# Optimization experiments

Measured on AMD Instinct MI355X. Metric: run time of the kernel, lower is better.

## Reference

```python
import jax, jax.numpy as jnp
import numpy as np

INPUT_SIZE = 1024
HIDDEN_SIZE = 1024
BATCH = 8192


def setup_inputs() -> dict:
    key = jax.random.key(0)
    ks = jax.random.split(key, 10)
    H, I, B = HIDDEN_SIZE, INPUT_SIZE, BATCH
    s = 1.0 / np.sqrt(H)  # scale params so activations stay in sane range
    return {
        "input": jax.random.normal(ks[0], (B, I), jnp.float32),
        "hx": jax.random.normal(ks[1], (B, H), jnp.float32),
        "cx": jax.random.normal(ks[2], (B, H), jnp.float32),
        "att": jax.random.normal(ks[3], (B, I), jnp.float32),
        "weight_ih": jax.random.normal(ks[4], (4 * H, I), jnp.float32) * s,
        "weight_hh": jax.random.normal(ks[5], (4 * H, H), jnp.float32) * s,
        "bias_ih": jax.random.normal(ks[6], (4 * H,), jnp.float32),
        "bias_hh": jax.random.normal(ks[7], (4 * H,), jnp.float32),
        "weight_att": jax.random.normal(ks[8], (2 * H, I), jnp.float32) * s,
        "bias_att": jax.random.normal(ks[9], (2 * H,), jnp.float32),
    }


def reference(input, hx, cx, att, weight_ih, weight_hh, bias_ih, bias_hh,
              weight_att, bias_att):
    H = weight_hh.shape[1]
    # gates: [B, 4H]
    gates = input @ weight_ih.T + bias_ih + hx @ weight_hh.T + bias_hh
    att_gates = att @ weight_att.T + bias_att  # [B, 2H]
    ingate, forgetgate, cellgate, outgate = jnp.split(gates, 4, axis=1)
    ingate_att, attgate = jnp.split(att_gates, 2, axis=1)
    ingate = jax.nn.sigmoid(ingate)
    forgetgate = jax.nn.sigmoid(forgetgate)
    cellgate = jnp.tanh(cellgate)
    ingate_att = jax.nn.sigmoid(ingate_att)
    attgate = jnp.tanh(attgate)
    outgate = jax.nn.sigmoid(outgate)
    cy = forgetgate * cx + ingate * cellgate + ingate_att * attgate
    hy = outgate * jnp.tanh(cy)
    return (hy, cy)
```

## Files before the change

kernel.cpp:

```cpp
#include <hip/hip_runtime.h>


typedef __attribute__((ext_vector_type(8))) __bf16 bf16x8;
typedef __attribute__((ext_vector_type(8))) unsigned short ushort8;
typedef __attribute__((ext_vector_type(4))) float f32x4;

#define AS1 __attribute__((address_space(1)))
#define AS3 __attribute__((address_space(3)))

__device__ __forceinline__ void gld16(const unsigned short* g, unsigned short* l) {
    __builtin_amdgcn_global_load_lds((const AS1 void*)g, (AS3 void*)l, 16, 0, 0);
}

__device__ __forceinline__ unsigned short f2bf(float f) {
    unsigned int u = __builtin_bit_cast(unsigned int, f);
    u += 0x7fffu + ((u >> 16) & 1u);
    return (unsigned short)(u >> 16);
}

__device__ __forceinline__ float sigmoidf_(float x) { return 1.f / (1.f + __expf(-x)); }
__device__ __forceinline__ float tanhf_(float x) {
    float e = __expf(-2.f * fabsf(x));
    float t = (1.f - e) / (1.f + e);
    return x >= 0.f ? t : -t;
}

__device__ __forceinline__ bf16x8 ldfrag(const unsigned short* p) {
    return __builtin_bit_cast(bf16x8, *(const ushort8*)p);
}

__global__ void cast_all_k(const float* __restrict__ input, const float* __restrict__ hx,
                           const float* __restrict__ att,   const float* __restrict__ w_ih,
                           const float* __restrict__ w_hh,  const float* __restrict__ w_att,
                           const float* __restrict__ b_ih,  const float* __restrict__ b_hh,
                           unsigned short* __restrict__ XH, unsigned short* __restrict__ ATTb,
                           unsigned short* __restrict__ W4, unsigned short* __restrict__ WA,
                           float* __restrict__ bias4)
{
    int gid = blockIdx.x * blockDim.x + threadIdx.x;
    if (gid < 4096) bias4[gid] = b_ih[gid] + b_hh[gid];
    const int total = 8912896;
    for (int i = gid; i < total; i += gridDim.x * blockDim.x) {
        const float* src; unsigned short* dst; int ld, off, rel;
        if (i < 2097152)      { src = input; dst = XH;   ld = 2048; off = 0;    rel = i; }
        else if (i < 4194304) { src = hx;    dst = XH;   ld = 2048; off = 1024; rel = i - 2097152; }
        else if (i < 6291456) { src = att;   dst = ATTb; ld = 1024; off = 0;    rel = i - 4194304; }
        else if (i < 7340032) { src = w_ih;  dst = W4;   ld = 2048; off = 0;    rel = i - 6291456; }
        else if (i < 8388608) { src = w_hh;  dst = W4;   ld = 2048; off = 1024; rel = i - 7340032; }
        else                  { src = w_att; dst = WA;   ld = 1024; off = 0;    rel = i - 8388608; }
        int e = rel * 4;
        int r = e >> 10, c = e & 1023;
        const float4 v = *(const float4*)(src + e);
        ushort4 p;
        p.x = f2bf(v.x); p.y = f2bf(v.y); p.z = f2bf(v.z); p.w = f2bf(v.w);
        *(ushort4*)(dst + r * ld + off + c) = p;
    }
}

__global__ __launch_bounds__(256, 2) void att_gemm_k(
    const unsigned short* __restrict__ ATT, const unsigned short* __restrict__ WA,
    const float* __restrict__ bias_att, float* __restrict__ attprod)
{
    __shared__ unsigned short As[128 * 32];
    __shared__ unsigned short Bs[128 * 32];
    const int tid  = threadIdx.x;
    const int wave = tid >> 6, lane = tid & 63;
    const int l15 = lane & 15, quad = lane >> 4;
    const int row0 = blockIdx.x * 128;
    const int n0   = blockIdx.y * 64;

    f32x4 acc[2][8];
    const f32x4 z = {0.f, 0.f, 0.f, 0.f};
#pragma unroll
    for (int i = 0; i < 2; ++i)
#pragma unroll
        for (int j = 0; j < 8; ++j) acc[i][j] = z;

    const int ar = tid >> 2;
    const int kp_sw = (tid & 3) ^ ((ar >> 1) & 3);
    const unsigned short* aG0 = ATT + (row0 + ar) * 1024 + kp_sw * 8;
    const unsigned short* aG1 = aG0 + 64 * 1024;
    const unsigned short* bG0 = WA + (n0 + ar) * 1024 + kp_sw * 8;
    const unsigned short* bG1 = WA + (1024 + n0 + ar) * 1024 + kp_sw * 8;
    unsigned short* aL0 = As + tid * 8;  unsigned short* aL1 = As + (tid + 256) * 8;
    unsigned short* bL0 = Bs + tid * 8;  unsigned short* bL1 = Bs + (tid + 256) * 8;

    const int sw8 = (quad ^ ((l15 >> 1) & 3)) * 8;
    const int aoff0 = (wave * 32 + l15) * 32 + sw8;
    const int aoff1 = aoff0 + 16 * 32;

    for (int kt = 0; kt < 32; ++kt) {
        gld16(aG0, aL0); gld16(aG1, aL1);
        gld16(bG0, bL0); gld16(bG1, bL1);
        aG0 += 32; aG1 += 32; bG0 += 32; bG1 += 32;
        __syncthreads();
        bf16x8 a0 = ldfrag(As + aoff0);
        bf16x8 a1 = ldfrag(As + aoff1);
#pragma unroll
        for (int cf = 0; cf < 8; ++cf) {
            bf16x8 b = ldfrag(Bs + (cf * 16 + l15) * 32 + sw8);
            acc[0][cf] = __builtin_amdgcn_mfma_f32_16x16x32_bf16(a0, b, acc[0][cf], 0, 0, 0);
            acc[1][cf] = __builtin_amdgcn_mfma_f32_16x16x32_bf16(a1, b, acc[1][cf], 0, 0, 0);
        }
        __syncthreads();
    }

    const int Rbase = row0 + wave * 32 + quad * 4;
#pragma unroll
    for (int rf = 0; rf < 2; ++rf)
#pragma unroll
        for (int jf = 0; jf < 4; ++jf) {
            int col = n0 + jf * 16 + l15;
            float b0 = bias_att[col], b1 = bias_att[1024 + col];
#pragma unroll
            for (int reg = 0; reg < 4; ++reg) {
                int R = Rbase + rf * 16 + reg;
                float ia = sigmoidf_(acc[rf][jf][reg] + b0);
                float ag = tanhf_(acc[rf][4 + jf][reg] + b1);
                attprod[R * 1024 + col] = ia * ag;
            }
        }
}

__global__ __launch_bounds__(256, 2) void main_gemm_k(
    const unsigned short* __restrict__ XH, const unsigned short* __restrict__ W4,
    const float* __restrict__ bias4, const float* __restrict__ attprod,
    const float* __restrict__ cx, float* __restrict__ out)
{
    __shared__ unsigned short As[128 * 32];
    __shared__ unsigned short Bs[128 * 32];
    const int tid  = threadIdx.x;
    const int wave = tid >> 6, lane = tid & 63;
    const int l15 = lane & 15, quad = lane >> 4;
    const int row0 = blockIdx.x * 128;
    const int n0   = blockIdx.y * 32;

    f32x4 acc[2][8];
    const f32x4 z = {0.f, 0.f, 0.f, 0.f};
#pragma unroll
    for (int i = 0; i < 2; ++i)
#pragma unroll
        for (int j = 0; j < 8; ++j) acc[i][j] = z;

    const int ar = tid >> 2;
    const int kp_sw = (tid & 3) ^ ((ar >> 1) & 3);
    const unsigned short* aG0 = XH + (row0 + ar) * 2048 + kp_sw * 8;
    const unsigned short* aG1 = aG0 + 64 * 2048;
    const unsigned short* bG0 = W4 + ((ar >> 5) * 1024 + n0 + (ar & 31)) * 2048 + kp_sw * 8;
    const unsigned short* bG1 = bG0 + 2 * 1024 * 2048;
    unsigned short* aL0 = As + tid * 8;  unsigned short* aL1 = As + (tid + 256) * 8;
    unsigned short* bL0 = Bs + tid * 8;  unsigned short* bL1 = Bs + (tid + 256) * 8;

    const int sw8 = (quad ^ ((l15 >> 1) & 3)) * 8;
    const int aoff0 = (wave * 32 + l15) * 32 + sw8;
    const int aoff1 = aoff0 + 16 * 32;

    for (int kt = 0; kt < 64; ++kt) {
        gld16(aG0, aL0); gld16(aG1, aL1);
        gld16(bG0, bL0); gld16(bG1, bL1);
        aG0 += 32; aG1 += 32; bG0 += 32; bG1 += 32;
        __syncthreads();
        bf16x8 a0 = ldfrag(As + aoff0);
        bf16x8 a1 = ldfrag(As + aoff1);
#pragma unroll
        for (int cf = 0; cf < 8; ++cf) {
            bf16x8 b = ldfrag(Bs + (cf * 16 + l15) * 32 + sw8);
            acc[0][cf] = __builtin_amdgcn_mfma_f32_16x16x32_bf16(a0, b, acc[0][cf], 0, 0, 0);
            acc[1][cf] = __builtin_amdgcn_mfma_f32_16x16x32_bf16(a1, b, acc[1][cf], 0, 0, 0);
        }
        __syncthreads();
    }

    const int Rbase = row0 + wave * 32 + quad * 4;
    const int CYOFF = 8192 * 1024;
#pragma unroll
    for (int rf = 0; rf < 2; ++rf)
#pragma unroll
        for (int jp = 0; jp < 2; ++jp) {
            int col = n0 + jp * 16 + l15;
            float bi  = bias4[col];
            float bff = bias4[1024 + col];
            float bg  = bias4[2048 + col];
            float bo  = bias4[3072 + col];
#pragma unroll
            for (int reg = 0; reg < 4; ++reg) {
                int R = Rbase + rf * 16 + reg;
                int off = R * 1024 + col;
                float ig = sigmoidf_(acc[rf][0 + jp][reg] + bi);
                float fg = sigmoidf_(acc[rf][2 + jp][reg] + bff);
                float gg = tanhf_(acc[rf][4 + jp][reg] + bg);
                float og = sigmoidf_(acc[rf][6 + jp][reg] + bo);
                float cyv = fg * cx[off] + ig * gg + attprod[off];
                float hyv = og * tanhf_(cyv);
                out[off] = hyv;
                out[CYOFF + off] = cyv;
            }
        }
}

extern "C" void kernel_launch(void* const* d_in, const int* in_sizes, int n_in,
                              void* d_out, int out_size, void* d_ws, size_t ws_size,
                              hipStream_t stream) {
    const float* input = (const float*)d_in[0];
    const float* hx    = (const float*)d_in[1];
    const float* cx    = (const float*)d_in[2];
    const float* att   = (const float*)d_in[3];
    const float* w_ih  = (const float*)d_in[4];
    const float* w_hh  = (const float*)d_in[5];
    const float* b_ih  = (const float*)d_in[6];
    const float* b_hh  = (const float*)d_in[7];
    const float* w_att = (const float*)d_in[8];
    const float* b_att = (const float*)d_in[9];
    float* out = (float*)d_out;

    char* ws = (char*)d_ws;
    unsigned short* XH   = (unsigned short*)(ws);
    unsigned short* ATTb = (unsigned short*)(ws + 33554432);
    unsigned short* W4   = (unsigned short*)(ws + 50331648);
    unsigned short* WA   = (unsigned short*)(ws + 67108864);
    float* bias4         = (float*)(ws + 71303168);
    float* attprod       = (float*)(ws + 71319552);

    cast_all_k<<<34816, 256, 0, stream>>>(input, hx, att, w_ih, w_hh, w_att,
                                          b_ih, b_hh, XH, ATTb, W4, WA, bias4);
    att_gemm_k<<<dim3(64, 16), 256, 0, stream>>>(ATTb, WA, b_att, attprod);
    main_gemm_k<<<dim3(64, 32), 256, 0, stream>>>(XH, W4, bias4, attprod, cx, out);
}
```

Measured before the change: 437.6 us.

## Fuse attention GEMM into main LSTM GEMM and widen cast vectorization

The separate attention GEMM kernel and its fp32 attprod intermediate are removed. The fused kernel runs a second K-loop over ATTb and WA and applies the sigmoid and tanh attention gates in the epilogue. This avoids writing and re-reading a 32MB fp32 buffer and saves one kernel launch. In exchange, each main-GEMM block recomputes its own attention tile, which lengthens each block's serial work. The cast kernel also now handles 8 elements per thread with 16-byte stores, using a quarter of the grid.

```diff
diff --git a/kernel.cpp b/kernel.cpp
--- a/kernel.cpp
+++ b/kernel.cpp
@@ -39,92 +39,30 @@
 {
     int gid = blockIdx.x * blockDim.x + threadIdx.x;
     if (gid < 4096) bias4[gid] = b_ih[gid] + b_hh[gid];
-    const int total = 8912896;
+    const int total = 4456448;
     for (int i = gid; i < total; i += gridDim.x * blockDim.x) {
         const float* src; unsigned short* dst; int ld, off, rel;
-        if (i < 2097152)      { src = input; dst = XH;   ld = 2048; off = 0;    rel = i; }
-        else if (i < 4194304) { src = hx;    dst = XH;   ld = 2048; off = 1024; rel = i - 2097152; }
-        else if (i < 6291456) { src = att;   dst = ATTb; ld = 1024; off = 0;    rel = i - 4194304; }
-        else if (i < 7340032) { src = w_ih;  dst = W4;   ld = 2048; off = 0;    rel = i - 6291456; }
-        else if (i < 8388608) { src = w_hh;  dst = W4;   ld = 2048; off = 1024; rel = i - 7340032; }
-        else                  { src = w_att; dst = WA;   ld = 1024; off = 0;    rel = i - 8388608; }
-        int e = rel * 4;
+        if (i < 1048576)      { src = input; dst = XH;   ld = 2048; off = 0;    rel = i; }
+        else if (i < 2097152) { src = hx;    dst = XH;   ld = 2048; off = 1024; rel = i - 1048576; }
+        else if (i < 3145728) { src = att;   dst = ATTb; ld = 1024; off = 0;    rel = i - 2097152; }
+        else if (i < 3670016) { src = w_ih;  dst = W4;   ld = 2048; off = 0;    rel = i - 3145728; }
+        else if (i < 4194304) { src = w_hh;  dst = W4;   ld = 2048; off = 1024; rel = i - 3670016; }
+        else                  { src = w_att; dst = WA;   ld = 1024; off = 0;    rel = i - 4194304; }
+        int e = rel * 8;
         int r = e >> 10, c = e & 1023;
-        const float4 v = *(const float4*)(src + e);
-        ushort4 p;
-        p.x = f2bf(v.x); p.y = f2bf(v.y); p.z = f2bf(v.z); p.w = f2bf(v.w);
-        *(ushort4*)(dst + r * ld + off + c) = p;
+        const float4 v0 = *(const float4*)(src + e);
+        const float4 v1 = *(const float4*)(src + e + 4);
+        ushort8 p;
+        p[0] = f2bf(v0.x); p[1] = f2bf(v0.y); p[2] = f2bf(v0.z); p[3] = f2bf(v0.w);
+        p[4] = f2bf(v1.x); p[5] = f2bf(v1.y); p[6] = f2bf(v1.z); p[7] = f2bf(v1.w);
+        *(ushort8*)(dst + r * ld + off + c) = p;
     }
 }
 
-__global__ __launch_bounds__(256, 2) void att_gemm_k(
-    const unsigned short* __restrict__ ATT, const unsigned short* __restrict__ WA,
-    const float* __restrict__ bias_att, float* __restrict__ attprod)
-{
-    __shared__ unsigned short As[128 * 32];
-    __shared__ unsigned short Bs[128 * 32];
-    const int tid  = threadIdx.x;
-    const int wave = tid >> 6, lane = tid & 63;
-    const int l15 = lane & 15, quad = lane >> 4;
-    const int row0 = blockIdx.x * 128;
-    const int n0   = blockIdx.y * 64;
-
-    f32x4 acc[2][8];
-    const f32x4 z = {0.f, 0.f, 0.f, 0.f};
-#pragma unroll
-    for (int i = 0; i < 2; ++i)
-#pragma unroll
-        for (int j = 0; j < 8; ++j) acc[i][j] = z;
-
-    const int ar = tid >> 2;
-    const int kp_sw = (tid & 3) ^ ((ar >> 1) & 3);
-    const unsigned short* aG0 = ATT + (row0 + ar) * 1024 + kp_sw * 8;
-    const unsigned short* aG1 = aG0 + 64 * 1024;
-    const unsigned short* bG0 = WA + (n0 + ar) * 1024 + kp_sw * 8;
-    const unsigned short* bG1 = WA + (1024 + n0 + ar) * 1024 + kp_sw * 8;
-    unsigned short* aL0 = As + tid * 8;  unsigned short* aL1 = As + (tid + 256) * 8;
-    unsigned short* bL0 = Bs + tid * 8;  unsigned short* bL1 = Bs + (tid + 256) * 8;
-
-    const int sw8 = (quad ^ ((l15 >> 1) & 3)) * 8;
-    const int aoff0 = (wave * 32 + l15) * 32 + sw8;
-    const int aoff1 = aoff0 + 16 * 32;
-
-    for (int kt = 0; kt < 32; ++kt) {
-        gld16(aG0, aL0); gld16(aG1, aL1);
-        gld16(bG0, bL0); gld16(bG1, bL1);
-        aG0 += 32; aG1 += 32; bG0 += 32; bG1 += 32;
-        __syncthreads();
-        bf16x8 a0 = ldfrag(As + aoff0);
-        bf16x8 a1 = ldfrag(As + aoff1);
-#pragma unroll
-        for (int cf = 0; cf < 8; ++cf) {
-            bf16x8 b = ldfrag(Bs + (cf * 16 + l15) * 32 + sw8);
-            acc[0][cf] = __builtin_amdgcn_mfma_f32_16x16x32_bf16(a0, b, acc[0][cf], 0, 0, 0);
-            acc[1][cf] = __builtin_amdgcn_mfma_f32_16x16x32_bf16(a1, b, acc[1][cf], 0, 0, 0);
-        }
-        __syncthreads();
-    }
-
-    const int Rbase = row0 + wave * 32 + quad * 4;
-#pragma unroll
-    for (int rf = 0; rf < 2; ++rf)
-#pragma unroll
-        for (int jf = 0; jf < 4; ++jf) {
-            int col = n0 + jf * 16 + l15;
-            float b0 = bias_att[col], b1 = bias_att[1024 + col];
-#pragma unroll
-            for (int reg = 0; reg < 4; ++reg) {
-                int R = Rbase + rf * 16 + reg;
-                float ia = sigmoidf_(acc[rf][jf][reg] + b0);
-                float ag = tanhf_(acc[rf][4 + jf][reg] + b1);
-                attprod[R * 1024 + col] = ia * ag;
-            }
-        }
-}
-
-__global__ __launch_bounds__(256, 2) void main_gemm_k(
+__global__ __launch_bounds__(256, 2) void fused_gemm_k(
     const unsigned short* __restrict__ XH, const unsigned short* __restrict__ W4,
-    const float* __restrict__ bias4, const float* __restrict__ attprod,
+    const unsigned short* __restrict__ ATTb, const unsigned short* __restrict__ WA,
+    const float* __restrict__ bias4, const float* __restrict__ bias_att,
     const float* __restrict__ cx, float* __restrict__ out)
 {
     __shared__ unsigned short As[128 * 32];
@@ -135,8 +73,8 @@
     const int row0 = blockIdx.x * 128;
     const int n0   = blockIdx.y * 32;
 
+    const f32x4 z = {0.f, 0.f, 0.f, 0.f};
     f32x4 acc[2][8];
-    const f32x4 z = {0.f, 0.f, 0.f, 0.f};
 #pragma unroll
     for (int i = 0; i < 2; ++i)
 #pragma unroll
@@ -144,10 +82,6 @@
 
     const int ar = tid >> 2;
     const int kp_sw = (tid & 3) ^ ((ar >> 1) & 3);
-    const unsigned short* aG0 = XH + (row0 + ar) * 2048 + kp_sw * 8;
-    const unsigned short* aG1 = aG0 + 64 * 2048;
-    const unsigned short* bG0 = W4 + ((ar >> 5) * 1024 + n0 + (ar & 31)) * 2048 + kp_sw * 8;
-    const unsigned short* bG1 = bG0 + 2 * 1024 * 2048;
     unsigned short* aL0 = As + tid * 8;  unsigned short* aL1 = As + (tid + 256) * 8;
     unsigned short* bL0 = Bs + tid * 8;  unsigned short* bL1 = Bs + (tid + 256) * 8;
 
@@ -155,20 +89,52 @@
     const int aoff0 = (wave * 32 + l15) * 32 + sw8;
     const int aoff1 = aoff0 + 16 * 32;
 
-    for (int kt = 0; kt < 64; ++kt) {
-        gld16(aG0, aL0); gld16(aG1, aL1);
-        gld16(bG0, bL0); gld16(bG1, bL1);
-        aG0 += 32; aG1 += 32; bG0 += 32; bG1 += 32;
-        __syncthreads();
-        bf16x8 a0 = ldfrag(As + aoff0);
-        bf16x8 a1 = ldfrag(As + aoff1);
+    {
+        const unsigned short* aG0 = XH + (row0 + ar) * 2048 + kp_sw * 8;
+        const unsigned short* aG1 = aG0 + 64 * 2048;
+        const unsigned short* bG0 = W4 + ((ar >> 5) * 1024 + n0 + (ar & 31)) * 2048 + kp_sw * 8;
+        const unsigned short* bG1 = bG0 + 2 * 1024 * 2048;
+        for (int kt = 0; kt < 64; ++kt) {
+            gld16(aG0, aL0); gld16(aG1, aL1);
+            gld16(bG0, bL0); gld16(bG1, bL1);
+            aG0 += 32; aG1 += 32; bG0 += 32; bG1 += 32;
+            __syncthreads();
+            bf16x8 a0 = ldfrag(As + aoff0);
+            bf16x8 a1 = ldfrag(As + aoff1);
 #pragma unroll
-        for (int cf = 0; cf < 8; ++cf) {
-            bf16x8 b = ldfrag(Bs + (cf * 16 + l15) * 32 + sw8);
-            acc[0][cf] = __builtin_amdgcn_mfma_f32_16x16x32_bf16(a0, b, acc[0][cf], 0, 0, 0);
-            acc[1][cf] = __builtin_amdgcn_mfma_f32_16x16x32_bf16(a1, b, acc[1][cf], 0, 0, 0);
+            for (int cf = 0; cf < 8; ++cf) {
+                bf16x8 b = ldfrag(Bs + (cf * 16 + l15) * 32 + sw8);
+                acc[0][cf] = __builtin_amdgcn_mfma_f32_16x16x32_bf16(a0, b, acc[0][cf], 0, 0, 0);
+                acc[1][cf] = __builtin_amdgcn_mfma_f32_16x16x32_bf16(a1, b, acc[1][cf], 0, 0, 0);
+            }
+            __syncthreads();
         }
-        __syncthreads();
+    }
+
+    f32x4 acc2[2][4];
+#pragma unroll
+    for (int i = 0; i < 2; ++i)
+#pragma unroll
+        for (int j = 0; j < 4; ++j) acc2[i][j] = z;
+    {
+        const unsigned short* aG0 = ATTb + (row0 + ar) * 1024 + kp_sw * 8;
+        const unsigned short* aG1 = aG0 + 64 * 1024;
+        const unsigned short* bG0 = WA + ((ar >> 5) * 1024 + n0 + (ar & 31)) * 1024 + kp_sw * 8;
+        for (int kt = 0; kt < 32; ++kt) {
+            gld16(aG0, aL0); gld16(aG1, aL1);
+            gld16(bG0, bL0);
+            aG0 += 32; aG1 += 32; bG0 += 32;
+            __syncthreads();
+            bf16x8 a0 = ldfrag(As + aoff0);
+            bf16x8 a1 = ldfrag(As + aoff1);
+#pragma unroll
+            for (int cf = 0; cf < 4; ++cf) {
+                bf16x8 b = ldfrag(Bs + (cf * 16 + l15) * 32 + sw8);
+                acc2[0][cf] = __builtin_amdgcn_mfma_f32_16x16x32_bf16(a0, b, acc2[0][cf], 0, 0, 0);
+                acc2[1][cf] = __builtin_amdgcn_mfma_f32_16x16x32_bf16(a1, b, acc2[1][cf], 0, 0, 0);
+            }
+            __syncthreads();
+        }
     }
 
     const int Rbase = row0 + wave * 32 + quad * 4;
@@ -182,6 +148,8 @@
             float bff = bias4[1024 + col];
             float bg  = bias4[2048 + col];
             float bo  = bias4[3072 + col];
+            float ba0 = bias_att[col];
+            float ba1 = bias_att[1024 + col];
 #pragma unroll
             for (int reg = 0; reg < 4; ++reg) {
                 int R = Rbase + rf * 16 + reg;
@@ -190,7 +158,9 @@
                 float fg = sigmoidf_(acc[rf][2 + jp][reg] + bff);
                 float gg = tanhf_(acc[rf][4 + jp][reg] + bg);
                 float og = sigmoidf_(acc[rf][6 + jp][reg] + bo);
-                float cyv = fg * cx[off] + ig * gg + attprod[off];
+                float ia = sigmoidf_(acc2[rf][0 + jp][reg] + ba0);
+                float ag = tanhf_(acc2[rf][2 + jp][reg] + ba1);
+                float cyv = fg * cx[off] + ig * gg + ia * ag;
                 float hyv = og * tanhf_(cyv);
                 out[off] = hyv;
                 out[CYOFF + off] = cyv;
@@ -219,10 +189,8 @@
     unsigned short* W4   = (unsigned short*)(ws + 50331648);
     unsigned short* WA   = (unsigned short*)(ws + 67108864);
     float* bias4         = (float*)(ws + 71303168);
-    float* attprod       = (float*)(ws + 71319552);
 
-    cast_all_k<<<34816, 256, 0, stream>>>(input, hx, att, w_ih, w_hh, w_att,
-                                          b_ih, b_hh, XH, ATTb, W4, WA, bias4);
-    att_gemm_k<<<dim3(64, 16), 256, 0, stream>>>(ATTb, WA, b_att, attprod);
-    main_gemm_k<<<dim3(64, 32), 256, 0, stream>>>(XH, W4, bias4, attprod, cx, out);
+    cast_all_k<<<8704, 256, 0, stream>>>(input, hx, att, w_ih, w_hh, w_att,
+                                         b_ih, b_hh, XH, ATTb, W4, WA, bias4);
+    fused_gemm_k<<<dim3(64, 32), 256, 0, stream>>>(XH, W4, ATTb, WA, bias4, b_att, cx, out);
 }
```

Measured after the change: 438.7 us. Within noise of the previous version (+0.3%).
